# Kernel tuning notes

Hardware: AMD Instinct MI355X
Metric: run time of the kernel (lower is better)

Reference implementation:

```python
import jax, jax.numpy as jnp
import numpy as np
import math

H = 768
NH = 12
D = H // NH


def setup_inputs() -> dict:
    key = jax.random.key(0)
    ks = jax.random.split(key, 13)
    B, S = 1, 384
    s = 0.02
    inp = {
        "hidden_states": jax.random.normal(ks[0], (B, S, H), jnp.float32),
        "attention_mask": jnp.zeros((B, 1, 1, S), jnp.float32),
        "pos_emb": jax.random.normal(ks[1], (B, S, S, H), jnp.float32),
        "Wq": jax.random.normal(ks[2], (H, H), jnp.float32) * s,
        "bq": jnp.zeros((H,), jnp.float32),
        "Wk": jax.random.normal(ks[3], (H, H), jnp.float32) * s,
        "bk": jnp.zeros((H,), jnp.float32),
        "Wv": jax.random.normal(ks[4], (H, H), jnp.float32) * s,
        "bv": jnp.zeros((H,), jnp.float32),
        "Wpk": jax.random.normal(ks[5], (H, H), jnp.float32) * s,
        "bpk": jnp.zeros((H,), jnp.float32),
        "Wpq": jax.random.normal(ks[6], (H, H), jnp.float32) * s,
        "bpq": jnp.zeros((H,), jnp.float32),
    }
    return inp


def reference(hidden_states, attention_mask, pos_emb,
              Wq, bq, Wk, bk, Wv, bv, Wpk, bpk, Wpq, bpq):
    B, S, Hd = hidden_states.shape
    split = lambda x: x.reshape(B, S, NH, D).transpose(0, 2, 1, 3)  # -> (B, h, S, d)
    q = split(hidden_states @ Wq + bq)
    k = split(hidden_states @ Wk + bk)
    v = split(hidden_states @ Wv + bv)

    # content-to-content
    c2c = jnp.einsum('bhid,bhjd->bhij', q, k)

    # per-pair position projections: (B,S,S,H) -> (B,S,S,h,d)
    pos_key = (pos_emb @ Wpk + bpk).reshape(B, S, S, NH, D)
    pos_query = (pos_emb @ Wpq + bpq).reshape(B, S, S, NH, D)

    # content-to-position: q[b,h,i,:] . pos_key[b,i,j,h,:]
    c2p = jnp.einsum('bhid,bijhd->bhij', q, pos_key)
    # position-to-content: pos_query[b,j,i,h,:] . k[b,h,j,:]
    p2c = jnp.einsum('bjihd,bhjd->bhij', pos_query, k)

    scores = (c2c + c2p + p2c) / math.sqrt(D) + attention_mask
    probs = jax.nn.softmax(scores, axis=-1)  # dropout is identity (p=0 / eval)
    ctx = jnp.einsum('bhij,bhjd->bhid', probs, v)
    return ctx.transpose(0, 2, 1, 3).reshape(B, S, Hd)
```

## Files before the change

kernel.cpp:

```cpp
#include <hip/hip_runtime.h>
#include <math.h>

#define SEQ 384
#define HDIM 768
#define NHEAD 12
#define DHEAD 64

__global__ __launch_bounds__(256)
void qkv_gemm(const float* __restrict__ X,
              const float* __restrict__ Wq, const float* __restrict__ bq,
              const float* __restrict__ Wk, const float* __restrict__ bk,
              const float* __restrict__ Wv, const float* __restrict__ bv,
              float* __restrict__ q, float* __restrict__ k, float* __restrict__ v)
{
    __shared__ float Xs[128 * 68];
    const int z = blockIdx.z;
    const float* W    = (z == 0) ? Wq : (z == 1) ? Wk : Wv;
    const float* bias = (z == 0) ? bq : (z == 1) ? bk : bv;
    float* out        = (z == 0) ? q  : (z == 1) ? k  : v;

    const int m0 = blockIdx.x * 64;
    const int n0 = blockIdx.y * 64;
    const int tid = threadIdx.x;
    const int ty = tid / 16, tx = tid % 16;

    const int lm = tid >> 2;
    const int lc = (tid & 3) * 4;

    float acc[4][4] = {};

    for (int k0 = 0; k0 < HDIM; k0 += 128) {
        float4 xa[8];
        #pragma unroll
        for (int it = 0; it < 8; it++)
            xa[it] = *(const float4*)&X[(size_t)(m0 + lm) * HDIM + k0 + it * 16 + lc];
        __syncthreads();
        #pragma unroll
        for (int it = 0; it < 8; it++) {
            const int kk = it * 16 + lc;
            Xs[(kk + 0) * 68 + lm] = xa[it].x;
            Xs[(kk + 1) * 68 + lm] = xa[it].y;
            Xs[(kk + 2) * 68 + lm] = xa[it].z;
            Xs[(kk + 3) * 68 + lm] = xa[it].w;
        }
        __syncthreads();
        const float* Wp = &W[(size_t)k0 * HDIM + n0 + 4 * tx];
        #pragma unroll 8
        for (int kk = 0; kk < 128; kk++) {
            float4 b4 = *(const float4*)&Wp[(size_t)kk * HDIM];
            float4 a4 = *(const float4*)&Xs[kk * 68 + 4 * ty];
            float a[4] = {a4.x, a4.y, a4.z, a4.w};
            float b[4] = {b4.x, b4.y, b4.z, b4.w};
            #pragma unroll
            for (int ia = 0; ia < 4; ia++)
                #pragma unroll
                for (int ib = 0; ib < 4; ib++)
                    acc[ia][ib] = fmaf(a[ia], b[ib], acc[ia][ib]);
        }
    }
    float4 bv4 = *(const float4*)&bias[n0 + 4 * tx];
    #pragma unroll
    for (int ia = 0; ia < 4; ia++) {
        float4 o;
        o.x = acc[ia][0] + bv4.x; o.y = acc[ia][1] + bv4.y;
        o.z = acc[ia][2] + bv4.z; o.w = acc[ia][3] + bv4.w;
        *(float4*)&out[(size_t)(m0 + 4 * ty + ia) * HDIM + n0 + 4 * tx] = o;
    }
}

__global__ __launch_bounds__(256)
void pos_proj(const float* __restrict__ q, const float* __restrict__ k,
              const float* __restrict__ Wpk, const float* __restrict__ Wpq,
              float* __restrict__ qp, float* __restrict__ kp)
{
    __shared__ float As[64][68];
    __shared__ float Bs[64][68];
    const int h = blockIdx.z % NHEAD;
    const int s = blockIdx.z / NHEAD;
    const float* Asrc = s ? k   : q;
    const float* Wsrc = s ? Wpq : Wpk;
    float* out        = s ? kp  : qp;

    const int i0 = blockIdx.x * 64, e0 = blockIdx.y * 64;
    const int tid = threadIdx.x;
    const int dg = tid % 16, row = tid / 16;

    #pragma unroll
    for (int r = 0; r < 4; r++) {
        const int rr = r * 16 + row;
        float4 a4 = *(const float4*)&Asrc[(size_t)(i0 + rr) * HDIM + h * 64 + dg * 4];
        float4 b4 = *(const float4*)&Wsrc[(size_t)(e0 + rr) * HDIM + h * 64 + dg * 4];
        As[dg * 4 + 0][rr] = a4.x; As[dg * 4 + 1][rr] = a4.y;
        As[dg * 4 + 2][rr] = a4.z; As[dg * 4 + 3][rr] = a4.w;
        Bs[dg * 4 + 0][rr] = b4.x; Bs[dg * 4 + 1][rr] = b4.y;
        Bs[dg * 4 + 2][rr] = b4.z; Bs[dg * 4 + 3][rr] = b4.w;
    }
    __syncthreads();

    const int ty = tid / 16, tx = tid % 16;
    float acc[4][4] = {};
    #pragma unroll 4
    for (int d = 0; d < 64; d++) {
        float4 a4 = *(const float4*)&As[d][4 * ty];
        float4 b4 = *(const float4*)&Bs[d][4 * tx];
        float a[4] = {a4.x, a4.y, a4.z, a4.w};
        float b[4] = {b4.x, b4.y, b4.z, b4.w};
        #pragma unroll
        for (int ia = 0; ia < 4; ia++)
            #pragma unroll
            for (int ib = 0; ib < 4; ib++)
                acc[ia][ib] = fmaf(a[ia], b[ib], acc[ia][ib]);
    }
    #pragma unroll
    for (int ia = 0; ia < 4; ia++) {
        float4 o = make_float4(acc[ia][0], acc[ia][1], acc[ia][2], acc[ia][3]);
        *(float4*)&out[((size_t)(i0 + 4 * ty + ia) * NHEAD + h) * HDIM + e0 + 4 * tx] = o;
    }
}

__global__ __launch_bounds__(256)
void cc_gemm(const float* __restrict__ q, const float* __restrict__ k,
             const float* __restrict__ bpq, const float* __restrict__ bpk,
             const float* __restrict__ mask, float* __restrict__ CC)
{
    __shared__ float Qs[64][68];
    __shared__ float Ks[64][68];
    __shared__ float cterm_s;
    const int h  = blockIdx.z;
    const int i0 = blockIdx.x * 64, j0 = blockIdx.y * 64;
    const int tid = threadIdx.x;
    const int dg = tid % 16, row = tid / 16;

    const float4 bq4 = *(const float4*)&bpq[h * 64 + dg * 4];
    const float4 bk4 = *(const float4*)&bpk[h * 64 + dg * 4];
    #pragma unroll
    for (int r = 0; r < 4; r++) {
        const int rr = r * 16 + row;
        float4 q4 = *(const float4*)&q[(size_t)(i0 + rr) * HDIM + h * 64 + dg * 4];
        float4 k4 = *(const float4*)&k[(size_t)(j0 + rr) * HDIM + h * 64 + dg * 4];
        Qs[dg * 4 + 0][rr] = q4.x + bq4.x; Qs[dg * 4 + 1][rr] = q4.y + bq4.y;
        Qs[dg * 4 + 2][rr] = q4.z + bq4.z; Qs[dg * 4 + 3][rr] = q4.w + bq4.w;
        Ks[dg * 4 + 0][rr] = k4.x + bk4.x; Ks[dg * 4 + 1][rr] = k4.y + bk4.y;
        Ks[dg * 4 + 2][rr] = k4.z + bk4.z; Ks[dg * 4 + 3][rr] = k4.w + bk4.w;
    }
    if (tid < 64) {
        float pc = bpq[h * 64 + tid] * bpk[h * 64 + tid];
        #pragma unroll
        for (int o = 32; o; o >>= 1) pc += __shfl_xor(pc, o);
        if (tid == 0) cterm_s = pc;
    }
    __syncthreads();

    const int ty = tid / 16, tx = tid % 16;
    float acc[4][4] = {};
    #pragma unroll 4
    for (int d = 0; d < 64; d++) {
        float4 a4 = *(const float4*)&Qs[d][4 * ty];
        float4 b4 = *(const float4*)&Ks[d][4 * tx];
        float a[4] = {a4.x, a4.y, a4.z, a4.w};
        float b[4] = {b4.x, b4.y, b4.z, b4.w};
        #pragma unroll
        for (int ia = 0; ia < 4; ia++)
            #pragma unroll
            for (int ib = 0; ib < 4; ib++)
                acc[ia][ib] = fmaf(a[ia], b[ib], acc[ia][ib]);
    }
    const float cterm = cterm_s;
    const float4 m4 = *(const float4*)&mask[j0 + 4 * tx];
    #pragma unroll
    for (int ia = 0; ia < 4; ia++) {
        float4 o;
        o.x = (acc[ia][0] - cterm) * 0.125f + m4.x;
        o.y = (acc[ia][1] - cterm) * 0.125f + m4.y;
        o.z = (acc[ia][2] - cterm) * 0.125f + m4.z;
        o.w = (acc[ia][3] - cterm) * 0.125f + m4.w;
        *(float4*)&CC[((size_t)h * SEQ + i0 + 4 * ty + ia) * SEQ + j0 + 4 * tx] = o;
    }
}

__global__ __launch_bounds__(256, 3)
void scores_pos(const float* __restrict__ pe, const float* __restrict__ qp,
                const float* __restrict__ kp,
                float* __restrict__ CC, float* __restrict__ P2T)
{
    __shared__ float lds[32 * 200];
    const int i    = blockIdx.x;
    const int jh   = blockIdx.y;
    const int tid  = threadIdx.x;
    const int lane = tid & 63;
    const int wave = tid >> 6;
    const int rgu = __builtin_amdgcn_readfirstlane(wave >> 1);
    const int esu = __builtin_amdgcn_readfirstlane(wave & 1);

    const float* pebase = pe + ((size_t)i * SEQ + jh * 192) * HDIM;
    const float* wb = (rgu ? kp : qp) + (size_t)i * NHEAD * HDIM;

    const int wr  = tid >> 3;
    const int wec = tid & 7;

    float acc[12][3] = {};
    float4 ga[6], gb[6];

    auto loadc = [&](float4* g, int c) {
        const int e0 = c * 32;
        #pragma unroll
        for (int rnd = 0; rnd < 3; rnd++) {
            const int jb = rnd * 64 + wr * 2;
            g[2 * rnd + 0] = *(const float4*)&pebase[(size_t)jb * HDIM + e0 + wec * 4];
            g[2 * rnd + 1] = *(const float4*)&pebase[(size_t)(jb + 1) * HDIM + e0 + wec * 4];
        }
    };
    auto writec = [&](const float4* g) {
        #pragma unroll
        for (int rnd = 0; rnd < 3; rnd++) {
            const int jb = rnd * 64 + wr * 2;
            const float4 g0 = g[2 * rnd], g1 = g[2 * rnd + 1];
            *(float2*)&lds[(wec * 4 + 0) * 200 + jb] = make_float2(g0.x, g1.x);
            *(float2*)&lds[(wec * 4 + 1) * 200 + jb] = make_float2(g0.y, g1.y);
            *(float2*)&lds[(wec * 4 + 2) * 200 + jb] = make_float2(g0.z, g1.z);
            *(float2*)&lds[(wec * 4 + 3) * 200 + jb] = make_float2(g0.w, g1.w);
        }
    };
    auto compute = [&](int c) {
        const float* wc = wb + c * 32 + esu * 16;
        #pragma unroll 4
        for (int ee = 0; ee < 16; ee++) {
            const int ei = esu * 16 + ee;
            float2 p2 = *(const float2*)&lds[ei * 200 + 2 * lane];
            float  p1 = lds[ei * 200 + 128 + lane];
            #pragma unroll
            for (int r = 0; r < 12; r++) {
                const float w = wc[r * HDIM + ee];
                acc[r][0] = fmaf(w, p2.x, acc[r][0]);
                acc[r][1] = fmaf(w, p2.y, acc[r][1]);
                acc[r][2] = fmaf(w, p1,   acc[r][2]);
            }
        }
    };

    loadc(ga, 0);
    #pragma unroll 1
    for (int cc = 0; cc < 12; cc++) {
        loadc(gb, 2 * cc + 1);
        __syncthreads();
        writec(ga);
        __syncthreads();
        if (cc < 11) loadc(ga, 2 * cc + 2);
        compute(2 * cc);
        __syncthreads();
        writec(gb);
        __syncthreads();
        compute(2 * cc + 1);
    }

    __syncthreads();
    if (esu == 1) {
        #pragma unroll
        for (int r = 0; r < 12; r++) {
            const int row = rgu * 12 + r;
            *(float2*)&lds[row * 200 + 2 * lane] = make_float2(acc[r][0], acc[r][1]);
            lds[row * 200 + 128 + lane] = acc[r][2];
        }
    }
    __syncthreads();
    if (esu == 0) {
        #pragma unroll
        for (int r = 0; r < 12; r++) {
            const int row = rgu * 12 + r;
            float2 o2 = *(const float2*)&lds[row * 200 + 2 * lane];
            float  o1 = lds[row * 200 + 128 + lane];
            o2.x += acc[r][0]; o2.y += acc[r][1]; o1 += acc[r][2];
            *(float2*)&lds[row * 200 + 2 * lane] = o2;
            lds[row * 200 + 128 + lane] = o1;
        }
    }
    __syncthreads();

    for (int t = tid; t < 24 * 48; t += 256) {
        const int row = t / 48;
        const int c4  = (t % 48) * 4;
        float4 o = *(const float4*)&lds[row * 200 + c4];
        o.x *= 0.125f; o.y *= 0.125f; o.z *= 0.125f; o.w *= 0.125f;
        if (row < 12) {
            float* dst = &CC[((size_t)row * SEQ + i) * SEQ + jh * 192 + c4];
            float4 c = *(const float4*)dst;
            c.x += o.x; c.y += o.y; c.z += o.z; c.w += o.w;
            *(float4*)dst = c;
        } else {
            *(float4*)&P2T[((size_t)(row - 12) * SEQ + i) * SEQ + jh * 192 + c4] = o;
        }
    }
}

__global__ __launch_bounds__(384)
void attn_out(const float* __restrict__ CC, const float* __restrict__ P2T,
              const float* __restrict__ v, float* __restrict__ out)
{
    const int i = blockIdx.x, h = blockIdx.y;
    const int tid = threadIdx.x;
    __shared__ float p_s[SEQ];
    __shared__ float redm[6], reds[6];
    __shared__ float redvf[24 * 64];

    float sc = CC[((size_t)h * SEQ + i) * SEQ + tid]
             + P2T[((size_t)h * SEQ + tid) * SEQ + i];

    const int lane = tid & 63, w = tid >> 6;
    float m = sc;
    #pragma unroll
    for (int o = 32; o; o >>= 1) m = fmaxf(m, __shfl_xor(m, o));
    if (lane == 0) redm[w] = m;
    __syncthreads();
    m = redm[0];
    #pragma unroll
    for (int t = 1; t < 6; t++) m = fmaxf(m, redm[t]);

    float p = __expf(sc - m);
    float sum = p;
    #pragma unroll
    for (int o = 32; o; o >>= 1) sum += __shfl_xor(sum, o);
    if (lane == 0) reds[w] = sum;
    p_s[tid] = p;
    __syncthreads();
    const float SUM = reds[0] + reds[1] + reds[2] + reds[3] + reds[4] + reds[5];

    const int dq = lane & 15, jsub = lane >> 4;
    const int j0 = w * 64;
    float4 av = make_float4(0.f, 0.f, 0.f, 0.f);
    #pragma unroll 8
    for (int jj = 0; jj < 16; jj++) {
        const int j = j0 + jj * 4 + jsub;
        float4 v4 = *(const float4*)&v[(size_t)j * HDIM + h * 64 + dq * 4];
        const float pj = p_s[j];
        av.x = fmaf(pj, v4.x, av.x); av.y = fmaf(pj, v4.y, av.y);
        av.z = fmaf(pj, v4.z, av.z); av.w = fmaf(pj, v4.w, av.w);
    }
    *(float4*)&redvf[(w * 4 + jsub) * 64 + dq * 4] = av;
    __syncthreads();
    if (tid < 64) {
        float o = 0.f;
        #pragma unroll
        for (int r = 0; r < 24; r++) o += redvf[r * 64 + tid];
        out[(size_t)i * HDIM + h * 64 + tid] = o / SUM;
    }
}

extern "C" void kernel_launch(void* const* d_in, const int* in_sizes, int n_in,
                              void* d_out, int out_size, void* d_ws, size_t ws_size,
                              hipStream_t stream)
{
    const float* hs   = (const float*)d_in[0];
    const float* mask = (const float*)d_in[1];
    const float* pe   = (const float*)d_in[2];
    const float* Wq   = (const float*)d_in[3];
    const float* bq   = (const float*)d_in[4];
    const float* Wk   = (const float*)d_in[5];
    const float* bk   = (const float*)d_in[6];
    const float* Wv   = (const float*)d_in[7];
    const float* bv   = (const float*)d_in[8];
    const float* Wpk  = (const float*)d_in[9];
    const float* bpk  = (const float*)d_in[10];
    const float* Wpq  = (const float*)d_in[11];
    const float* bpq  = (const float*)d_in[12];

    float* ws = (float*)d_ws;
    const size_t SZ_QKV = (size_t)SEQ * HDIM;
    const size_t SZ_QP  = (size_t)SEQ * NHEAD * HDIM;
    const size_t SZ_SC  = (size_t)NHEAD * SEQ * SEQ;
    float* q   = ws;
    float* k   = q  + SZ_QKV;
    float* v   = k  + SZ_QKV;
    float* qp  = v  + SZ_QKV;
    float* kp  = qp + SZ_QP;
    float* P2T = kp + SZ_QP;
    float* CC  = P2T + SZ_SC;

    qkv_gemm<<<dim3(6, 12, 3), 256, 0, stream>>>(hs, Wq, bq, Wk, bk, Wv, bv, q, k, v);
    cc_gemm<<<dim3(6, 6, 12), 256, 0, stream>>>(q, k, bpq, bpk, mask, CC);
    pos_proj<<<dim3(6, 12, 24), 256, 0, stream>>>(q, k, Wpk, Wpq, qp, kp);
    scores_pos<<<dim3(SEQ, 2), 256, 0, stream>>>(pe, qp, kp, CC, P2T);
    attn_out<<<dim3(SEQ, NHEAD), 384, 0, stream>>>(CC, P2T, v, (float*)d_out);
}
```

Before: 791.1 us.

## Merge projection launches, drop CC read-modify-write, add tiled transpose fold kernel

Merges the content-to-content GEMM and the position projection GEMM into one launch by branching on blockIdx.z. scores_pos now writes its c2p block to a separate buffer instead of doing a read-modify-write on CC. A new tiled kernel transposes P2T through LDS and sums CC, A1 and the transposed P2T into one score matrix S, so attn_out reads coalesced rows instead of strided P2T columns. The cost is an extra launch plus roughly two more score-sized buffers of memory traffic, in exchange for removing the uncoalesced column reads.

```diff
diff --git a/kernel.cpp b/kernel.cpp
--- a/kernel.cpp
+++ b/kernel.cpp
@@ -69,119 +69,115 @@
 }
 
 __global__ __launch_bounds__(256)
-void pos_proj(const float* __restrict__ q, const float* __restrict__ k,
+void proj_all(const float* __restrict__ q, const float* __restrict__ k,
               const float* __restrict__ Wpk, const float* __restrict__ Wpq,
-              float* __restrict__ qp, float* __restrict__ kp)
+              const float* __restrict__ bpq, const float* __restrict__ bpk,
+              const float* __restrict__ mask,
+              float* __restrict__ qp, float* __restrict__ kp,
+              float* __restrict__ CC)
 {
     __shared__ float As[64][68];
     __shared__ float Bs[64][68];
-    const int h = blockIdx.z % NHEAD;
-    const int s = blockIdx.z / NHEAD;
-    const float* Asrc = s ? k   : q;
-    const float* Wsrc = s ? Wpq : Wpk;
-    float* out        = s ? kp  : qp;
-
-    const int i0 = blockIdx.x * 64, e0 = blockIdx.y * 64;
+    __shared__ float cterm_s;
+    const int z = blockIdx.z;
     const int tid = threadIdx.x;
     const int dg = tid % 16, row = tid / 16;
-
-    #pragma unroll
-    for (int r = 0; r < 4; r++) {
-        const int rr = r * 16 + row;
-        float4 a4 = *(const float4*)&Asrc[(size_t)(i0 + rr) * HDIM + h * 64 + dg * 4];
-        float4 b4 = *(const float4*)&Wsrc[(size_t)(e0 + rr) * HDIM + h * 64 + dg * 4];
-        As[dg * 4 + 0][rr] = a4.x; As[dg * 4 + 1][rr] = a4.y;
-        As[dg * 4 + 2][rr] = a4.z; As[dg * 4 + 3][rr] = a4.w;
-        Bs[dg * 4 + 0][rr] = b4.x; Bs[dg * 4 + 1][rr] = b4.y;
-        Bs[dg * 4 + 2][rr] = b4.z; Bs[dg * 4 + 3][rr] = b4.w;
-    }
-    __syncthreads();
-
     const int ty = tid / 16, tx = tid % 16;
-    float acc[4][4] = {};
-    #pragma unroll 4
-    for (int d = 0; d < 64; d++) {
-        float4 a4 = *(const float4*)&As[d][4 * ty];
-        float4 b4 = *(const float4*)&Bs[d][4 * tx];
-        float a[4] = {a4.x, a4.y, a4.z, a4.w};
-        float b[4] = {b4.x, b4.y, b4.z, b4.w};
-        #pragma unroll
-        for (int ia = 0; ia < 4; ia++)
+
+    if (z < 24) {
+        const int h = z % NHEAD;
+        const int s = z / NHEAD;
+        const float* Asrc = s ? k   : q;
+        const float* Wsrc = s ? Wpq : Wpk;
+        float* out        = s ? kp  : qp;
+        const int i0 = blockIdx.x * 64, e0 = blockIdx.y * 64;
+
+        #pragma unroll
+        for (int r = 0; r < 4; r++) {
+            const int rr = r * 16 + row;
+            float4 a4 = *(const float4*)&Asrc[(size_t)(i0 + rr) * HDIM + h * 64 + dg * 4];
+            float4 b4 = *(const float4*)&Wsrc[(size_t)(e0 + rr) * HDIM + h * 64 + dg * 4];
+            As[dg * 4 + 0][rr] = a4.x; As[dg * 4 + 1][rr] = a4.y;
+            As[dg * 4 + 2][rr] = a4.z; As[dg * 4 + 3][rr] = a4.w;
+            Bs[dg * 4 + 0][rr] = b4.x; Bs[dg * 4 + 1][rr] = b4.y;
+            Bs[dg * 4 + 2][rr] = b4.z; Bs[dg * 4 + 3][rr] = b4.w;
+        }
+        __syncthreads();
+
+        float acc[4][4] = {};
+        #pragma unroll 4
+        for (int d = 0; d < 64; d++) {
+            float4 a4 = *(const float4*)&As[d][4 * ty];
+            float4 b4 = *(const float4*)&Bs[d][4 * tx];
+            float a[4] = {a4.x, a4.y, a4.z, a4.w};
+            float b[4] = {b4.x, b4.y, b4.z, b4.w};
             #pragma unroll
-            for (int ib = 0; ib < 4; ib++)
-                acc[ia][ib] = fmaf(a[ia], b[ib], acc[ia][ib]);
-    }
-    #pragma unroll
-    for (int ia = 0; ia < 4; ia++) {
-        float4 o = make_float4(acc[ia][0], acc[ia][1], acc[ia][2], acc[ia][3]);
-        *(float4*)&out[((size_t)(i0 + 4 * ty + ia) * NHEAD + h) * HDIM + e0 + 4 * tx] = o;
-    }
-}
-
-__global__ __launch_bounds__(256)
-void cc_gemm(const float* __restrict__ q, const float* __restrict__ k,
-             const float* __restrict__ bpq, const float* __restrict__ bpk,
-             const float* __restrict__ mask, float* __restrict__ CC)
-{
-    __shared__ float Qs[64][68];
-    __shared__ float Ks[64][68];
-    __shared__ float cterm_s;
-    const int h  = blockIdx.z;
-    const int i0 = blockIdx.x * 64, j0 = blockIdx.y * 64;
-    const int tid = threadIdx.x;
-    const int dg = tid % 16, row = tid / 16;
-
-    const float4 bq4 = *(const float4*)&bpq[h * 64 + dg * 4];
-    const float4 bk4 = *(const float4*)&bpk[h * 64 + dg * 4];
-    #pragma unroll
-    for (int r = 0; r < 4; r++) {
-        const int rr = r * 16 + row;
-        float4 q4 = *(const float4*)&q[(size_t)(i0 + rr) * HDIM + h * 64 + dg * 4];
-        float4 k4 = *(const float4*)&k[(size_t)(j0 + rr) * HDIM + h * 64 + dg * 4];
-        Qs[dg * 4 + 0][rr] = q4.x + bq4.x; Qs[dg * 4 + 1][rr] = q4.y + bq4.y;
-        Qs[dg * 4 + 2][rr] = q4.z + bq4.z; Qs[dg * 4 + 3][rr] = q4.w + bq4.w;
-        Ks[dg * 4 + 0][rr] = k4.x + bk4.x; Ks[dg * 4 + 1][rr] = k4.y + bk4.y;
-        Ks[dg * 4 + 2][rr] = k4.z + bk4.z; Ks[dg * 4 + 3][rr] = k4.w + bk4.w;
-    }
-    if (tid < 64) {
-        float pc = bpq[h * 64 + tid] * bpk[h * 64 + tid];
-        #pragma unroll
-        for (int o = 32; o; o >>= 1) pc += __shfl_xor(pc, o);
-        if (tid == 0) cterm_s = pc;
-    }
-    __syncthreads();
-
-    const int ty = tid / 16, tx = tid % 16;
-    float acc[4][4] = {};
-    #pragma unroll 4
-    for (int d = 0; d < 64; d++) {
-        float4 a4 = *(const float4*)&Qs[d][4 * ty];
-        float4 b4 = *(const float4*)&Ks[d][4 * tx];
-        float a[4] = {a4.x, a4.y, a4.z, a4.w};
-        float b[4] = {b4.x, b4.y, b4.z, b4.w};
-        #pragma unroll
-        for (int ia = 0; ia < 4; ia++)
+            for (int ia = 0; ia < 4; ia++)
+                #pragma unroll
+                for (int ib = 0; ib < 4; ib++)
+                    acc[ia][ib] = fmaf(a[ia], b[ib], acc[ia][ib]);
+        }
+        #pragma unroll
+        for (int ia = 0; ia < 4; ia++) {
+            float4 o = make_float4(acc[ia][0], acc[ia][1], acc[ia][2], acc[ia][3]);
+            *(float4*)&out[((size_t)(i0 + 4 * ty + ia) * NHEAD + h) * HDIM + e0 + 4 * tx] = o;
+        }
+    } else {
+        if (blockIdx.y >= 6) return;
+        const int h  = z - 24;
+        const int i0 = blockIdx.x * 64, j0 = blockIdx.y * 64;
+
+        const float4 bq4 = *(const float4*)&bpq[h * 64 + dg * 4];
+        const float4 bk4 = *(const float4*)&bpk[h * 64 + dg * 4];
+        #pragma unroll
+        for (int r = 0; r < 4; r++) {
+            const int rr = r * 16 + row;
+            float4 q4 = *(const float4*)&q[(size_t)(i0 + rr) * HDIM + h * 64 + dg * 4];
+            float4 k4 = *(const float4*)&k[(size_t)(j0 + rr) * HDIM + h * 64 + dg * 4];
+            As[dg * 4 + 0][rr] = q4.x + bq4.x; As[dg * 4 + 1][rr] = q4.y + bq4.y;
+            As[dg * 4 + 2][rr] = q4.z + bq4.z; As[dg * 4 + 3][rr] = q4.w + bq4.w;
+            Bs[dg * 4 + 0][rr] = k4.x + bk4.x; Bs[dg * 4 + 1][rr] = k4.y + bk4.y;
+            Bs[dg * 4 + 2][rr] = k4.z + bk4.z; Bs[dg * 4 + 3][rr] = k4.w + bk4.w;
+        }
+        if (tid < 64) {
+            float pc = bpq[h * 64 + tid] * bpk[h * 64 + tid];
             #pragma unroll
-            for (int ib = 0; ib < 4; ib++)
-                acc[ia][ib] = fmaf(a[ia], b[ib], acc[ia][ib]);
-    }
-    const float cterm = cterm_s;
-    const float4 m4 = *(const float4*)&mask[j0 + 4 * tx];
-    #pragma unroll
-    for (int ia = 0; ia < 4; ia++) {
-        float4 o;
-        o.x = (acc[ia][0] - cterm) * 0.125f + m4.x;
-        o.y = (acc[ia][1] - cterm) * 0.125f + m4.y;
-        o.z = (acc[ia][2] - cterm) * 0.125f + m4.z;
-        o.w = (acc[ia][3] - cterm) * 0.125f + m4.w;
-        *(float4*)&CC[((size_t)h * SEQ + i0 + 4 * ty + ia) * SEQ + j0 + 4 * tx] = o;
+            for (int o = 32; o; o >>= 1) pc += __shfl_xor(pc, o);
+            if (tid == 0) cterm_s = pc;
+        }
+        __syncthreads();
+
+        float acc[4][4] = {};
+        #pragma unroll 4
+        for (int d = 0; d < 64; d++) {
+            float4 a4 = *(const float4*)&As[d][4 * ty];
+            float4 b4 = *(const float4*)&Bs[d][4 * tx];
+            float a[4] = {a4.x, a4.y, a4.z, a4.w};
+            float b[4] = {b4.x, b4.y, b4.z, b4.w};
+            #pragma unroll
+            for (int ia = 0; ia < 4; ia++)
+                #pragma unroll
+                for (int ib = 0; ib < 4; ib++)
+                    acc[ia][ib] = fmaf(a[ia], b[ib], acc[ia][ib]);
+        }
+        const float cterm = cterm_s;
+        const float4 m4 = *(const float4*)&mask[j0 + 4 * tx];
+        #pragma unroll
+        for (int ia = 0; ia < 4; ia++) {
+            float4 o;
+            o.x = (acc[ia][0] - cterm) * 0.125f + m4.x;
+            o.y = (acc[ia][1] - cterm) * 0.125f + m4.y;
+            o.z = (acc[ia][2] - cterm) * 0.125f + m4.z;
+            o.w = (acc[ia][3] - cterm) * 0.125f + m4.w;
+            *(float4*)&CC[((size_t)h * SEQ + i0 + 4 * ty + ia) * SEQ + j0 + 4 * tx] = o;
+        }
     }
 }
 
 __global__ __launch_bounds__(256, 3)
 void scores_pos(const float* __restrict__ pe, const float* __restrict__ qp,
                 const float* __restrict__ kp,
-                float* __restrict__ CC, float* __restrict__ P2T)
+                float* __restrict__ A1, float* __restrict__ P2T)
 {
     __shared__ float lds[32 * 200];
     const int i    = blockIdx.x;
@@ -281,20 +277,51 @@
         const int c4  = (t % 48) * 4;
         float4 o = *(const float4*)&lds[row * 200 + c4];
         o.x *= 0.125f; o.y *= 0.125f; o.z *= 0.125f; o.w *= 0.125f;
-        if (row < 12) {
-            float* dst = &CC[((size_t)row * SEQ + i) * SEQ + jh * 192 + c4];
-            float4 c = *(const float4*)dst;
-            c.x += o.x; c.y += o.y; c.z += o.z; c.w += o.w;
-            *(float4*)dst = c;
-        } else {
-            *(float4*)&P2T[((size_t)(row - 12) * SEQ + i) * SEQ + jh * 192 + c4] = o;
-        }
+        float* dst = (row < 12)
+            ? &A1[((size_t)row * SEQ + i) * SEQ + jh * 192 + c4]
+            : &P2T[((size_t)(row - 12) * SEQ + i) * SEQ + jh * 192 + c4];
+        *(float4*)dst = o;
+    }
+}
+
+__global__ __launch_bounds__(256)
+void fold_transpose(const float* __restrict__ CC, const float* __restrict__ A1,
+                    const float* __restrict__ P2T, float* __restrict__ S)
+{
+    __shared__ float T[64 * 65];
+    const int h  = blockIdx.z;
+    const int i0 = blockIdx.x * 64, j0 = blockIdx.y * 64;
+    const int tid = threadIdx.x;
+    const int c = tid % 16, r = tid / 16;
+
+    #pragma unroll
+    for (int p = 0; p < 4; p++) {
+        const int jr = p * 16 + r;
+        float4 t4 = *(const float4*)&P2T[((size_t)h * SEQ + j0 + jr) * SEQ + i0 + 4 * c];
+        T[(4 * c + 0) * 65 + jr] = t4.x;
+        T[(4 * c + 1) * 65 + jr] = t4.y;
+        T[(4 * c + 2) * 65 + jr] = t4.z;
+        T[(4 * c + 3) * 65 + jr] = t4.w;
+    }
+    __syncthreads();
+    #pragma unroll
+    for (int p = 0; p < 4; p++) {
+        const int ir = p * 16 + r;
+        const size_t off = ((size_t)h * SEQ + i0 + ir) * SEQ + j0 + 4 * c;
+        float4 cc4 = *(const float4*)&CC[off];
+        float4 a4  = *(const float4*)&A1[off];
+        float4 o;
+        o.x = cc4.x + a4.x + T[ir * 65 + 4 * c + 0];
+        o.y = cc4.y + a4.y + T[ir * 65 + 4 * c + 1];
+        o.z = cc4.z + a4.z + T[ir * 65 + 4 * c + 2];
+        o.w = cc4.w + a4.w + T[ir * 65 + 4 * c + 3];
+        *(float4*)&S[off] = o;
     }
 }
 
 __global__ __launch_bounds__(384)
-void attn_out(const float* __restrict__ CC, const float* __restrict__ P2T,
-              const float* __restrict__ v, float* __restrict__ out)
+void attn_out(const float* __restrict__ S, const float* __restrict__ v,
+              float* __restrict__ out)
 {
     const int i = blockIdx.x, h = blockIdx.y;
     const int tid = threadIdx.x;
@@ -302,8 +329,7 @@
     __shared__ float redm[6], reds[6];
     __shared__ float redvf[24 * 64];
 
-    float sc = CC[((size_t)h * SEQ + i) * SEQ + tid]
-             + P2T[((size_t)h * SEQ + tid) * SEQ + i];
+    float sc = S[((size_t)h * SEQ + i) * SEQ + tid];
 
     const int lane = tid & 63, w = tid >> 6;
     float m = sc;
@@ -372,12 +398,15 @@
     float* v   = k  + SZ_QKV;
     float* qp  = v  + SZ_QKV;
     float* kp  = qp + SZ_QP;
-    float* P2T = kp + SZ_QP;
+    float* A1  = kp + SZ_QP;
+    float* P2T = A1 + SZ_SC;
     float* CC  = P2T + SZ_SC;
+    float* S   = CC + SZ_SC;
 
     qkv_gemm<<<dim3(6, 12, 3), 256, 0, stream>>>(hs, Wq, bq, Wk, bk, Wv, bv, q, k, v);
-    cc_gemm<<<dim3(6, 6, 12), 256, 0, stream>>>(q, k, bpq, bpk, mask, CC);
-    pos_proj<<<dim3(6, 12, 24), 256, 0, stream>>>(q, k, Wpk, Wpq, qp, kp);
-    scores_pos<<<dim3(SEQ, 2), 256, 0, stream>>>(pe, qp, kp, CC, P2T);
-    attn_out<<<dim3(SEQ, NHEAD), 384, 0, stream>>>(CC, P2T, v, (float*)d_out);
-}
+    proj_all<<<dim3(6, 12, 36), 256, 0, stream>>>(q, k, Wpk, Wpq, bpq, bpk, mask,
+                                                  qp, kp, CC);
+    scores_pos<<<dim3(SEQ, 2), 256, 0, stream>>>(pe, qp, kp, A1, P2T);
+    fold_transpose<<<dim3(6, 6, 12), 256, 0, stream>>>(CC, A1, P2T, S);
+    attn_out<<<dim3(SEQ, NHEAD), 384, 0, stream>>>(S, v, (float*)d_out);
+}
```

Measured after the change: 790.4 us. Within noise of the previous version (-0.1%).
